# Optimization experiments

Measured on AMD Instinct MI355X. Metric: run time of the kernel, lower is better.

## Reference

```python
import jax, jax.numpy as jnp
import numpy as np

B, S, D = 2, 2048, 1024
H = 16
DK = D // H
SCALE = 1.0 / np.sqrt(DK)

def setup_inputs() -> dict:
    key = jax.random.key(0)
    ks = jax.random.split(key, 11)
    std = 1.0 / np.sqrt(D)
    return {
        "query": jax.random.normal(ks[0], (B, S, D), jnp.float32),
        "key":   jax.random.normal(ks[1], (B, S, D), jnp.float32),
        "value": jax.random.normal(ks[2], (B, S, D), jnp.float32),
        "Wq": jax.random.normal(ks[3], (D, H * DK), jnp.float32) * std,
        "bq": jnp.zeros((H * DK,), jnp.float32),
        "Wk": jax.random.normal(ks[4], (D, H * DK), jnp.float32) * std,
        "bk": jnp.zeros((H * DK,), jnp.float32),
        "Wv": jax.random.normal(ks[5], (D, H * DK), jnp.float32) * std,
        "bv": jnp.zeros((H * DK,), jnp.float32),
        "Wo": jax.random.normal(ks[6], (D, D), jnp.float32) * std,
        "bo": jnp.zeros((D,), jnp.float32),
    }

def reference(query, key, value, Wq, bq, Wk, bk, Wv, bv, Wo, bo):
    b, s, _ = query.shape
    # projections -> [b, s, h, d_k]
    q = (query @ Wq + bq).reshape(b, s, H, DK)
    k = (key   @ Wk + bk).reshape(b, s, H, DK)
    v = (value @ Wv + bv).reshape(b, s, H, DK)
    # scores [b, i, j, h]
    scores = jnp.einsum('bihd,bjhd->bijh', q, k) * SCALE
    attn = jax.nn.softmax(scores, axis=2)  # softmax over key dim j
    # dropout rate 0.0 (eval mode) -> identity
    x = jnp.einsum('bijh,bjhd->bihd', attn, v).reshape(b, s, H * DK)
    return x @ Wo + bo
```

## Files before the change

### kernel.cpp

```cpp
#include <hip/hip_runtime.h>
#include <hip/hip_bf16.h>
#include <math.h>
#include <stdint.h>

constexpr int Bb = 2, Ss = 2048, Dd = 1024, Hh = 16;
constexpr int Mm = Bb * Ss;
constexpr int Nn = Dd;
constexpr int Kk = Dd;
constexpr float QSCALE = 0.125f * 1.44269504088896340736f;

typedef unsigned short ushort_t;
typedef __attribute__((ext_vector_type(8))) short bf16x8;
typedef __attribute__((ext_vector_type(4))) float f32x4;
typedef __attribute__((ext_vector_type(16))) float f32x16;

#if __has_builtin(__builtin_amdgcn_exp2f)
#define EXP2F(x) __builtin_amdgcn_exp2f(x)
#else
#define EXP2F(x) exp2f(x)
#endif

__device__ __forceinline__ ushort_t f2bf(float f) {
  union { float f; unsigned u; } v; v.f = f;
  return (ushort_t)((v.u + 0x7fff + ((v.u >> 16) & 1)) >> 16);
}

__device__ __forceinline__ void load16_lds(const void* g, void* l) {
  __builtin_amdgcn_global_load_lds(
      (const __attribute__((address_space(1))) void*)(uintptr_t)g,
      (__attribute__((address_space(3))) void*)(uint32_t)(uintptr_t)l, 16, 0, 0);
}

__global__ __launch_bounds__(256) void convert_qkv(
    const float* __restrict__ q, const float* __restrict__ k,
    const float* __restrict__ v, ushort_t* __restrict__ out) {
  const int z = blockIdx.z;
  const float* src = (z == 0) ? q : (z == 1) ? k : v;
  ushort_t* dst = out + (size_t)z * Mm * Kk;
  const size_t idx = ((size_t)blockIdx.x * 256 + threadIdx.x) * 4;
  const float4 val = *(const float4*)(src + idx);
  ushort4 o;
  o.x = f2bf(val.x); o.y = f2bf(val.y); o.z = f2bf(val.z); o.w = f2bf(val.w);
  *(ushort4*)(dst + idx) = o;
}

__global__ __launch_bounds__(256) void transpose_w(
    const float* __restrict__ Wq, const float* __restrict__ Wk,
    const float* __restrict__ Wv, const float* __restrict__ Wo,
    ushort_t* __restrict__ Wt) {
  const int z = blockIdx.z;
  const float* W = (z == 0) ? Wq : (z == 1) ? Wk : (z == 2) ? Wv : Wo;
  ushort_t* out = Wt + (size_t)z * Kk * Nn;
  __shared__ float t[64][65];
  const int tid = threadIdx.x;
  const int n0 = blockIdx.x * 64, k0 = blockIdx.y * 64;
  const int lr = tid >> 4, lc = (tid & 15) * 4;
#pragma unroll
  for (int i = 0; i < 4; i++) {
    const int r = lr + i * 16;
    const float4 v = *(const float4*)(W + (size_t)(k0 + r) * Nn + n0 + lc);
    t[r][lc] = v.x; t[r][lc + 1] = v.y; t[r][lc + 2] = v.z; t[r][lc + 3] = v.w;
  }
  __syncthreads();
  const int n = tid >> 2, kc = (tid & 3) * 16;
  ushort_t tmp[16];
#pragma unroll
  for (int j = 0; j < 16; j++) tmp[j] = f2bf(t[kc + j][n]);
  ushort_t* op = out + (size_t)(n0 + n) * Kk + k0 + kc;
  ((uint4*)op)[0] = ((uint4*)tmp)[0];
  ((uint4*)op)[1] = ((uint4*)tmp)[1];
}

__global__ __launch_bounds__(256) void transpose_v(
    const ushort_t* __restrict__ Vp, ushort_t* __restrict__ Vt) {
  __shared__ ushort_t t[64][68];
  const int tid = threadIdx.x;
  const int s0 = blockIdx.x * 64, h = blockIdx.y, b = blockIdx.z;
  const int lr = tid >> 4, lc = (tid & 15) * 4;
#pragma unroll
  for (int i = 0; i < 4; i++) {
    const int r = lr + i * 16;
    const ushort4 v =
        *(const ushort4*)(Vp + (size_t)(b * Ss + s0 + r) * Dd + h * 64 + lc);
    *(ushort4*)&t[r][lc] = v;
  }
  __syncthreads();
  const int d = tid >> 2, sc = (tid & 3) * 16;
  ushort_t tmp[16];
#pragma unroll
  for (int j = 0; j < 16; j++) tmp[j] = t[sc + j][d];
  ushort_t* op = Vt + ((size_t)b * Dd + h * 64 + d) * Ss + s0 + sc;
  ((uint4*)op)[0] = ((uint4*)tmp)[0];
  ((uint4*)op)[1] = ((uint4*)tmp)[1];
}

template <int BN, bool OUT_BF16>
__global__ __launch_bounds__(256) void gemm_mfma(
    const ushort_t* __restrict__ Abase, size_t a_stride,
    const ushort_t* __restrict__ Wbase, size_t w_stride,
    const float* __restrict__ bias0, const float* __restrict__ bias1,
    const float* __restrict__ bias2, void* __restrict__ Cbase, size_t c_stride,
    float scale_z0) {
  constexpr int BM = 128, BK = 32;
  constexpr int WM = (BN == 128) ? 64 : 32;
  constexpr int MT_ = WM / 32;
  constexpr int NT_ = 2;
  __shared__ ushort_t As[BM * BK];
  __shared__ ushort_t Bs[BN * BK];
  const int tid = threadIdx.x, lane = tid & 63, wid = tid >> 6;
  const int z = blockIdx.z;
  const ushort_t* A = Abase + (size_t)z * a_stride;
  const ushort_t* Wt = Wbase + (size_t)z * w_stride;
  const float* bias = (z == 0) ? bias0 : (z == 1) ? bias1 : bias2;
  const float sc = (z == 0) ? scale_z0 : 1.0f;
  const int m0 = blockIdx.y * BM, n0 = blockIdx.x * BN;
  const int wm = (BN == 128) ? (wid >> 1) * 64 : wid * 32;
  const int wn = (BN == 128) ? (wid & 1) * 64 : 0;
  const int r32 = lane & 31, half = lane >> 5;
  const int srow = lane >> 2;
  const int scol = (lane & 3) * 8;

  f32x16 acc[MT_][NT_];
#pragma unroll
  for (int m = 0; m < MT_; m++)
#pragma unroll
    for (int n = 0; n < NT_; n++)
#pragma unroll
      for (int i = 0; i < 16; i++) acc[m][n][i] = 0.f;

  for (int k0 = 0; k0 < Kk; k0 += BK) {
    __syncthreads();
#pragma unroll
    for (int i = 0; i < BM / 64; i++) {
      const int I = wid * (BM / 64) + i;
      load16_lds(A + (size_t)(m0 + I * 16 + srow) * Kk + k0 + scol, As + I * 512);
    }
#pragma unroll
    for (int i = 0; i < BN / 64; i++) {
      const int I = wid * (BN / 64) + i;
      load16_lds(Wt + (size_t)(n0 + I * 16 + srow) * Kk + k0 + scol, Bs + I * 512);
    }
    __syncthreads();
    bf16x8 af[MT_][2], bfr[NT_][2];
#pragma unroll
    for (int m = 0; m < MT_; m++)
#pragma unroll
      for (int kin = 0; kin < 2; kin++)
        af[m][kin] = *(const bf16x8*)(
            As + (wm + m * 32 + r32) * BK + kin * 16 + half * 8);
#pragma unroll
    for (int n = 0; n < NT_; n++)
#pragma unroll
      for (int kin = 0; kin < 2; kin++)
        bfr[n][kin] = *(const bf16x8*)(
            Bs + (wn + n * 32 + r32) * BK + kin * 16 + half * 8);
#pragma unroll
    for (int kin = 0; kin < 2; kin++)
#pragma unroll
      for (int m = 0; m < MT_; m++)
#pragma unroll
        for (int n = 0; n < NT_; n++)
          acc[m][n] = __builtin_amdgcn_mfma_f32_32x32x16_bf16(
              af[m][kin], bfr[n][kin], acc[m][n], 0, 0, 0);
  }

#pragma unroll
  for (int m = 0; m < MT_; m++) {
#pragma unroll
    for (int n = 0; n < NT_; n++) {
      const int gc = n0 + wn + n * 32 + r32;
      const float bv = bias[gc];
#pragma unroll
      for (int g = 0; g < 4; g++) {
#pragma unroll
        for (int r = 0; r < 4; r++) {
          const int gr = m0 + wm + m * 32 + r + 4 * half + 8 * g;
          const float v = (acc[m][n][g * 4 + r] + bv) * sc;
          if (OUT_BF16)
            ((ushort_t*)Cbase)[(size_t)z * c_stride + (size_t)gr * Nn + gc] = f2bf(v);
          else
            ((float*)Cbase)[(size_t)z * c_stride + (size_t)gr * Nn + gc] = v;
        }
      }
    }
  }
}

__global__ __launch_bounds__(256) void flash_mfma(
    const ushort_t* __restrict__ Qp, const ushort_t* __restrict__ Kp,
    const ushort_t* __restrict__ Vt, ushort_t* __restrict__ Xp) {
  __shared__ ushort_t Ks[64 * 64];
  __shared__ ushort_t Vts[64 * 64];
  __shared__ ushort_t Ps[64 * 72];
  const int tid = threadIdx.x, lane = tid & 63, wid = tid >> 6;
  const int qt = blockIdx.x, h = blockIdx.y, b = blockIdx.z;
  const int quad = lane >> 4, r16 = lane & 15;
  const int row8 = lane >> 3;
  const int colsw = ((lane & 7) ^ (row8 & 7)) * 8;
  const int swz = r16 & 7;

  const int qrow = wid * 16 + r16;
  const ushort_t* Qg = Qp + ((size_t)(b * Ss + qt * 64)) * Dd + h * 64;
  const ushort_t* Kg = Kp + ((size_t)b * Ss) * Dd + h * 64;
  const ushort_t* Vg = Vt + ((size_t)b * Dd + h * 64) * Ss;

  bf16x8 qf[2];
#pragma unroll
  for (int ks = 0; ks < 2; ks++)
    qf[ks] = *(const bf16x8*)(Qg + (size_t)qrow * Dd + ks * 32 + quad * 8);

  f32x4 acc[4];
  float rs = 0.f;
#pragma unroll
  for (int mt = 0; mt < 4; mt++) acc[mt] = f32x4{0.f, 0.f, 0.f, 0.f};

  for (int kt = 0; kt < Ss / 64; kt++) {
    __syncthreads();
#pragma unroll
    for (int i = 0; i < 2; i++) {
      const int I = wid * 2 + i;
      load16_lds(Kg + (size_t)(kt * 64 + I * 8 + row8) * Dd + colsw, Ks + I * 512);
      load16_lds(Vg + (size_t)(I * 8 + row8) * Ss + kt * 64 + colsw, Vts + I * 512);
    }
    __syncthreads();

    f32x4 sacc[4];
#pragma unroll
    for (int mm = 0; mm < 4; mm++) sacc[mm] = f32x4{0.f, 0.f, 0.f, 0.f};
#pragma unroll
    for (int ks = 0; ks < 2; ks++) {
      const int ko = ((ks * 4 + quad) ^ swz) * 8;
      bf16x8 kf[4];
#pragma unroll
      for (int mm = 0; mm < 4; mm++)
        kf[mm] = *(const bf16x8*)(Ks + (mm * 16 + r16) * 64 + ko);
#pragma unroll
      for (int mm = 0; mm < 4; mm++)
        sacc[mm] = __builtin_amdgcn_mfma_f32_16x16x32_bf16(
            kf[mm], qf[ks], sacc[mm], 0, 0, 0);
    }

#pragma unroll
    for (int mm = 0; mm < 4; mm++) {
      float p0 = EXP2F(sacc[mm][0]), p1 = EXP2F(sacc[mm][1]);
      float p2 = EXP2F(sacc[mm][2]), p3 = EXP2F(sacc[mm][3]);
      rs += (p0 + p1) + (p2 + p3);
      union { __hip_bfloat162 hh; unsigned u; } lo, hi;
      lo.hh = __float22bfloat162_rn(make_float2(p0, p1));
      hi.hh = __float22bfloat162_rn(make_float2(p2, p3));
      *(uint2*)(Ps + qrow * 72 + mm * 16 + quad * 4) = make_uint2(lo.u, hi.u);
    }

#pragma unroll
    for (int ks = 0; ks < 2; ks++) {
      const int ko = ((ks * 4 + quad) ^ swz) * 8;
      bf16x8 vf[4];
#pragma unroll
      for (int mt = 0; mt < 4; mt++)
        vf[mt] = *(const bf16x8*)(Vts + (mt * 16 + r16) * 64 + ko);
      const bf16x8 pf = *(const bf16x8*)(Ps + qrow * 72 + ks * 32 + quad * 8);
#pragma unroll
      for (int mt = 0; mt < 4; mt++)
        acc[mt] = __builtin_amdgcn_mfma_f32_16x16x32_bf16(
            vf[mt], pf, acc[mt], 0, 0, 0);
    }
  }

  rs += __shfl_xor(rs, 16, 64);
  rs += __shfl_xor(rs, 32, 64);
  const float inv = 1.0f / rs;

#pragma unroll
  for (int mt = 0; mt < 4; mt++) {
    ushort4 o;
    o.x = f2bf(acc[mt][0] * inv);
    o.y = f2bf(acc[mt][1] * inv);
    o.z = f2bf(acc[mt][2] * inv);
    o.w = f2bf(acc[mt][3] * inv);
    *(ushort4*)(Xp + (size_t)(b * Ss + qt * 64 + qrow) * Dd +
                h * 64 + mt * 16 + quad * 4) = o;
  }
}

extern "C" void kernel_launch(void* const* d_in, const int* in_sizes, int n_in,
                              void* d_out, int out_size, void* d_ws,
                              size_t ws_size, hipStream_t stream) {
  const float* q  = (const float*)d_in[0];
  const float* k  = (const float*)d_in[1];
  const float* v  = (const float*)d_in[2];
  const float* Wq = (const float*)d_in[3];
  const float* bq = (const float*)d_in[4];
  const float* Wk = (const float*)d_in[5];
  const float* bk = (const float*)d_in[6];
  const float* Wv = (const float*)d_in[7];
  const float* bv = (const float*)d_in[8];
  const float* Wo = (const float*)d_in[9];
  const float* bo = (const float*)d_in[10];

  ushort_t* ws = (ushort_t*)d_ws;
  const size_t MD = (size_t)Mm * Kk;
  const size_t KN = (size_t)Kk * Nn;
  ushort_t* qkvb = ws;
  ushort_t* Wt   = ws + 3 * MD;
  ushort_t* QKVp = Wt + 4 * KN;
  ushort_t* Vtp  = QKVp + 3 * MD;
  ushort_t* Xp   = qkvb;

  convert_qkv<<<dim3(4096, 1, 3), 256, 0, stream>>>(q, k, v, qkvb);
  transpose_w<<<dim3(16, 16, 4), 256, 0, stream>>>(Wq, Wk, Wv, Wo, Wt);
  gemm_mfma<128, true><<<dim3(Nn / 128, Mm / 128, 3), 256, 0, stream>>>(
      qkvb, MD, Wt, KN, bq, bk, bv, QKVp, MD, QSCALE);
  transpose_v<<<dim3(Ss / 64, Hh, Bb), 256, 0, stream>>>(QKVp + 2 * MD, Vtp);
  flash_mfma<<<dim3(Ss / 64, Hh, Bb), 256, 0, stream>>>(QKVp, QKVp + MD, Vtp, Xp);
  gemm_mfma<64, false><<<dim3(Nn / 64, Mm / 128, 1), 256, 0, stream>>>(
      Xp, 0, Wt + 3 * KN, 0, bo, bo, bo, d_out, 0, 1.0f);
}
```

Measured before the change: 243.6 us.

## Fuse fp32-to-bf16 input conversion into QKV GEMM and switch to 16x16x32 MFMA

```diff
diff --git a/kernel.cpp b/kernel.cpp
--- a/kernel.cpp
+++ b/kernel.cpp
@@ -12,7 +12,6 @@
 typedef unsigned short ushort_t;
 typedef __attribute__((ext_vector_type(8))) short bf16x8;
 typedef __attribute__((ext_vector_type(4))) float f32x4;
-typedef __attribute__((ext_vector_type(16))) float f32x16;
 
 #if __has_builtin(__builtin_amdgcn_exp2f)
 #define EXP2F(x) __builtin_amdgcn_exp2f(x)
@@ -29,19 +28,6 @@
   __builtin_amdgcn_global_load_lds(
       (const __attribute__((address_space(1))) void*)(uintptr_t)g,
       (__attribute__((address_space(3))) void*)(uint32_t)(uintptr_t)l, 16, 0, 0);
-}
-
-__global__ __launch_bounds__(256) void convert_qkv(
-    const float* __restrict__ q, const float* __restrict__ k,
-    const float* __restrict__ v, ushort_t* __restrict__ out) {
-  const int z = blockIdx.z;
-  const float* src = (z == 0) ? q : (z == 1) ? k : v;
-  ushort_t* dst = out + (size_t)z * Mm * Kk;
-  const size_t idx = ((size_t)blockIdx.x * 256 + threadIdx.x) * 4;
-  const float4 val = *(const float4*)(src + idx);
-  ushort4 o;
-  o.x = f2bf(val.x); o.y = f2bf(val.y); o.z = f2bf(val.z); o.w = f2bf(val.w);
-  *(ushort4*)(dst + idx) = o;
 }
 
 __global__ __launch_bounds__(256) void transpose_w(
@@ -94,46 +80,60 @@
   ((uint4*)op)[1] = ((uint4*)tmp)[1];
 }
 
-template <int BN, bool OUT_BF16>
+template <int BN, bool OUT_BF16, bool A_FP32>
 __global__ __launch_bounds__(256) void gemm_mfma(
-    const ushort_t* __restrict__ Abase, size_t a_stride,
-    const ushort_t* __restrict__ Wbase, size_t w_stride,
-    const float* __restrict__ bias0, const float* __restrict__ bias1,
-    const float* __restrict__ bias2, void* __restrict__ Cbase, size_t c_stride,
-    float scale_z0) {
+    const void* __restrict__ A0, const void* __restrict__ A1,
+    const void* __restrict__ A2, const ushort_t* __restrict__ Wbase,
+    size_t w_stride, const float* __restrict__ bias0,
+    const float* __restrict__ bias1, const float* __restrict__ bias2,
+    void* __restrict__ Cbase, size_t c_stride, float scale_z0) {
   constexpr int BM = 128, BK = 32;
+  constexpr int ASTR = A_FP32 ? 40 : 32;
   constexpr int WM = (BN == 128) ? 64 : 32;
-  constexpr int MT_ = WM / 32;
-  constexpr int NT_ = 2;
-  __shared__ ushort_t As[BM * BK];
+  constexpr int MT_ = WM / 16, NT_ = 4;
+  __shared__ ushort_t As[BM * ASTR];
   __shared__ ushort_t Bs[BN * BK];
   const int tid = threadIdx.x, lane = tid & 63, wid = tid >> 6;
   const int z = blockIdx.z;
-  const ushort_t* A = Abase + (size_t)z * a_stride;
+  const void* Av = (z == 0) ? A0 : (z == 1) ? A1 : A2;
   const ushort_t* Wt = Wbase + (size_t)z * w_stride;
   const float* bias = (z == 0) ? bias0 : (z == 1) ? bias1 : bias2;
   const float sc = (z == 0) ? scale_z0 : 1.0f;
   const int m0 = blockIdx.y * BM, n0 = blockIdx.x * BN;
   const int wm = (BN == 128) ? (wid >> 1) * 64 : wid * 32;
   const int wn = (BN == 128) ? (wid & 1) * 64 : 0;
-  const int r32 = lane & 31, half = lane >> 5;
+  const int quad = lane >> 4, r16 = lane & 15;
   const int srow = lane >> 2;
   const int scol = (lane & 3) * 8;
 
-  f32x16 acc[MT_][NT_];
+  f32x4 acc[MT_][NT_];
 #pragma unroll
   for (int m = 0; m < MT_; m++)
 #pragma unroll
-    for (int n = 0; n < NT_; n++)
-#pragma unroll
-      for (int i = 0; i < 16; i++) acc[m][n][i] = 0.f;
+    for (int n = 0; n < NT_; n++) acc[m][n] = f32x4{0.f, 0.f, 0.f, 0.f};
 
   for (int k0 = 0; k0 < Kk; k0 += BK) {
     __syncthreads();
-#pragma unroll
-    for (int i = 0; i < BM / 64; i++) {
-      const int I = wid * (BM / 64) + i;
-      load16_lds(A + (size_t)(m0 + I * 16 + srow) * Kk + k0 + scol, As + I * 512);
+    if (A_FP32) {
+      const float* A = (const float*)Av;
+#pragma unroll
+      for (int i = 0; i < 4; i++) {
+        const int idx = i * 256 + tid;
+        const int row = idx >> 3, c = idx & 7;
+        const float4 v4 =
+            *(const float4*)(A + (size_t)(m0 + row) * Kk + k0 + c * 4);
+        ushort4 o;
+        o.x = f2bf(v4.x); o.y = f2bf(v4.y); o.z = f2bf(v4.z); o.w = f2bf(v4.w);
+        *(ushort4*)(As + row * ASTR + c * 4) = o;
+      }
+    } else {
+      const ushort_t* A = (const ushort_t*)Av;
+#pragma unroll
+      for (int i = 0; i < BM / 64; i++) {
+        const int I = wid * (BM / 64) + i;
+        load16_lds(A + (size_t)(m0 + I * 16 + srow) * Kk + k0 + scol,
+                   As + I * 512);
+      }
     }
 #pragma unroll
     for (int i = 0; i < BN / 64; i++) {
@@ -141,46 +141,35 @@
       load16_lds(Wt + (size_t)(n0 + I * 16 + srow) * Kk + k0 + scol, Bs + I * 512);
     }
     __syncthreads();
-    bf16x8 af[MT_][2], bfr[NT_][2];
+    bf16x8 af[MT_], bfr[NT_];
 #pragma unroll
     for (int m = 0; m < MT_; m++)
-#pragma unroll
-      for (int kin = 0; kin < 2; kin++)
-        af[m][kin] = *(const bf16x8*)(
-            As + (wm + m * 32 + r32) * BK + kin * 16 + half * 8);
+      af[m] = *(const bf16x8*)(As + (wm + m * 16 + r16) * ASTR + quad * 8);
 #pragma unroll
     for (int n = 0; n < NT_; n++)
-#pragma unroll
-      for (int kin = 0; kin < 2; kin++)
-        bfr[n][kin] = *(const bf16x8*)(
-            Bs + (wn + n * 32 + r32) * BK + kin * 16 + half * 8);
-#pragma unroll
-    for (int kin = 0; kin < 2; kin++)
-#pragma unroll
-      for (int m = 0; m < MT_; m++)
-#pragma unroll
-        for (int n = 0; n < NT_; n++)
-          acc[m][n] = __builtin_amdgcn_mfma_f32_32x32x16_bf16(
-              af[m][kin], bfr[n][kin], acc[m][n], 0, 0, 0);
+      bfr[n] = *(const bf16x8*)(Bs + (wn + n * 16 + r16) * BK + quad * 8);
+#pragma unroll
+    for (int m = 0; m < MT_; m++)
+#pragma unroll
+      for (int n = 0; n < NT_; n++)
+        acc[m][n] =
+            __builtin_amdgcn_mfma_f32_16x16x32_bf16(af[m], bfr[n], acc[m][n], 0, 0, 0);
   }
 
 #pragma unroll
   for (int m = 0; m < MT_; m++) {
 #pragma unroll
     for (int n = 0; n < NT_; n++) {
-      const int gc = n0 + wn + n * 32 + r32;
+      const int gc = n0 + wn + n * 16 + r16;
       const float bv = bias[gc];
 #pragma unroll
-      for (int g = 0; g < 4; g++) {
-#pragma unroll
-        for (int r = 0; r < 4; r++) {
-          const int gr = m0 + wm + m * 32 + r + 4 * half + 8 * g;
-          const float v = (acc[m][n][g * 4 + r] + bv) * sc;
-          if (OUT_BF16)
-            ((ushort_t*)Cbase)[(size_t)z * c_stride + (size_t)gr * Nn + gc] = f2bf(v);
-          else
-            ((float*)Cbase)[(size_t)z * c_stride + (size_t)gr * Nn + gc] = v;
-        }
+      for (int r = 0; r < 4; r++) {
+        const int gr = m0 + wm + m * 16 + quad * 4 + r;
+        const float v = (acc[m][n][r] + bv) * sc;
+        if (OUT_BF16)
+          ((ushort_t*)Cbase)[(size_t)z * c_stride + (size_t)gr * Nn + gc] = f2bf(v);
+        else
+          ((float*)Cbase)[(size_t)z * c_stride + (size_t)gr * Nn + gc] = v;
       }
     }
   }
@@ -300,18 +289,16 @@
   ushort_t* ws = (ushort_t*)d_ws;
   const size_t MD = (size_t)Mm * Kk;
   const size_t KN = (size_t)Kk * Nn;
-  ushort_t* qkvb = ws;
-  ushort_t* Wt   = ws + 3 * MD;
-  ushort_t* QKVp = Wt + 4 * KN;
+  ushort_t* Wt   = ws;
+  ushort_t* QKVp = ws + 4 * KN;
   ushort_t* Vtp  = QKVp + 3 * MD;
-  ushort_t* Xp   = qkvb;
-
-  convert_qkv<<<dim3(4096, 1, 3), 256, 0, stream>>>(q, k, v, qkvb);
+  ushort_t* Xp   = Vtp + MD;
+
   transpose_w<<<dim3(16, 16, 4), 256, 0, stream>>>(Wq, Wk, Wv, Wo, Wt);
-  gemm_mfma<128, true><<<dim3(Nn / 128, Mm / 128, 3), 256, 0, stream>>>(
-      qkvb, MD, Wt, KN, bq, bk, bv, QKVp, MD, QSCALE);
+  gemm_mfma<128, true, true><<<dim3(Nn / 128, Mm / 128, 3), 256, 0, stream>>>(
+      q, k, v, Wt, KN, bq, bk, bv, QKVp, MD, QSCALE);
   transpose_v<<<dim3(Ss / 64, Hh, Bb), 256, 0, stream>>>(QKVp + 2 * MD, Vtp);
   flash_mfma<<<dim3(Ss / 64, Hh, Bb), 256, 0, stream>>>(QKVp, QKVp + MD, Vtp, Xp);
-  gemm_mfma<64, false><<<dim3(Nn / 64, Mm / 128, 1), 256, 0, stream>>>(
-      Xp, 0, Wt + 3 * KN, 0, bo, bo, bo, d_out, 0, 1.0f);
-}
+  gemm_mfma<64, false, false><<<dim3(Nn / 64, Mm / 128, 1), 256, 0, stream>>>(
+      Xp, Xp, Xp, Wt + 3 * KN, 0, bo, bo, bo, d_out, 0, 1.0f);
+}
```

New measurement: 259.7 us. 6.6% more time.
